# Kernel tuning notes

Hardware: AMD Instinct MI355X
Metric: run time of the kernel (lower is better)

## Reference

```python
import jax, jax.numpy as jnp
import numpy as np

IN_FF = 7  # joints
MASK = np.ones(9, dtype=np.float32)  # [P(3), RPY sin/cos (6)]


def _mlp(x, params):
    # params: list of (W, b); sigmoid after every layer except the last (predict)
    h = x
    for W, b in params[:-1]:
        h = jax.nn.sigmoid(h @ W + b)
    W, b = params[-1]
    return h @ W + b


def _rpy_head(x, params):
    # FeedForwardNet_RPY forward: y -> [sin(y0), cos(y1)], angle = atan2(sin, cos)
    y = _mlp(x, params)
    s = jnp.sin(y[..., 0])
    c = jnp.cos(y[..., 1])
    ang = jnp.arctan2(s, c)
    return jnp.stack([s, c, ang], axis=-1)  # (..., 3)


def setup_inputs():
    key = jax.random.key(0)
    ks = jax.random.split(key, 26)
    m = 16384
    d = {"x": jax.random.normal(ks[0], (m, 2 * IN_FF), jnp.float32)}

    def lin(k, fi, fo, name, i):
        k1, k2 = jax.random.split(k)
        lim = 1.0 / np.sqrt(fi)  # torch Linear default init
        d[name + "_W" + str(i)] = jax.random.uniform(k1, (fi, fo), jnp.float32, -lim, lim)
        d[name + "_b" + str(i)] = jax.random.uniform(k2, (fo,), jnp.float32, -lim, lim)

    idx = 1
    for name, dims in [("pos", [7, 512, 512, 3]), ("roll", [7, 256, 256, 2]),
                       ("pitch", [7, 256, 256, 2]), ("yaw", [7, 256, 256, 2])]:
        for i in range(3):
            lin(ks[idx], dims[i], dims[i + 1], name, i)
            idx += 1
    return d


def _forward(x, pos_p, roll_p, pitch_p, yaw_p):
    mask = jnp.asarray(MASK)
    M_P, M_RPY = mask[:3], mask[3:]
    q, qdot = x[:, :IN_FF], x[:, IN_FF:]

    # position net: forward + per-sample Jacobian (exact, replaces the autograd loop)
    P = _mlp(q, pos_p)                                          # (m, 3)
    J_P = jax.vmap(jax.jacfwd(lambda z: _mlp(z, pos_p)))(q)     # (m, 3, 7)
    vel = jnp.einsum("moi,mi->mo", J_P, qdot)                   # bmm(J_P, jointVels)
    P = P * M_P
    vel = vel * M_P

    heads = []
    for p in (roll_p, pitch_p, yaw_p):
        f = lambda z, p=p: _rpy_head(z, p)
        y = f(q)                                # (m, 3): [sin, cos, angle]
        J = jax.vmap(jax.jacfwd(f))(q)          # (m, 3, 7)
        v = jnp.einsum("moi,mi->mo", J[:, :2, :], qdot)  # (m, 2)
        heads.append((y, J, v))
    (yR, JR, vR), (yPi, JPi, vPi), (yY, JY, vY) = heads

    # order: [roll_sin, pitch_sin, yaw_sin, roll_cos, pitch_cos, yaw_cos]
    RPY = jnp.stack([yR[:, 0], yPi[:, 0], yY[:, 0], yR[:, 1], yPi[:, 1], yY[:, 1]], axis=1) * M_RPY
    vel_RPY = jnp.stack([vR[:, 0], vPi[:, 0], vY[:, 0], vR[:, 1], vPi[:, 1], vY[:, 1]], axis=1) * M_RPY
    J_RPY = jnp.stack([JR[:, 0], JPi[:, 0], JY[:, 0], JR[:, 1], JPi[:, 1], JY[:, 1]], axis=1)  # (m,6,7)

    out = jnp.concatenate([P, RPY, vel, vel_RPY], axis=1)            # (m, 18)
    J_tot = jnp.concatenate([J_P, J_RPY], axis=1)                    # (m, 9, 7)
    out_angles = jnp.concatenate([P, yR[:, 2:3], yPi[:, 2:3], yY[:, 2:3]], axis=1)       # (m, 6)
    J_tot_angles = jnp.concatenate([J_P, JR[:, 2:3], JPi[:, 2:3], JY[:, 2:3]], axis=1)   # (m, 6, 7)
    return out, J_tot, out_angles, J_tot_angles


def reference(x, pos_W0, pos_b0, pos_W1, pos_b1, pos_W2, pos_b2,
              roll_W0, roll_b0, roll_W1, roll_b1, roll_W2, roll_b2,
              pitch_W0, pitch_b0, pitch_W1, pitch_b1, pitch_W2, pitch_b2,
              yaw_W0, yaw_b0, yaw_W1, yaw_b1, yaw_W2, yaw_b2):
    pos_p = [(pos_W0, pos_b0), (pos_W1, pos_b1), (pos_W2, pos_b2)]
    roll_p = [(roll_W0, roll_b0), (roll_W1, roll_b1), (roll_W2, roll_b2)]
    pitch_p = [(pitch_W0, pitch_b0), (pitch_W1, pitch_b1), (pitch_W2, pitch_b2)]
    yaw_p = [(yaw_W0, yaw_b0), (yaw_W1, yaw_b1), (yaw_W2, yaw_b2)]
    return _forward(x, pos_p, roll_p, pitch_p, yaw_p)
```

## Files before the change

### kernel.cpp

```cpp
#include <hip/hip_runtime.h>
#include <math.h>

typedef __attribute__((ext_vector_type(8))) short short8;
typedef __attribute__((ext_vector_type(4))) float floatx4;
typedef __attribute__((ext_vector_type(2))) float floatx2;
typedef __attribute__((ext_vector_type(2))) unsigned uint2v;

__device__ __forceinline__ float sig(float z) { return 1.0f / (1.0f + __expf(-z)); }

__device__ __forceinline__ unsigned short f2bf(float f) {
    unsigned u = __float_as_uint(f);
    u = (u + 0x7FFFu + ((u >> 16) & 1u)) >> 16;
    return (unsigned short)u;
}

__device__ __forceinline__ unsigned cvtpk_bf16(float lo, float hi) {
    unsigned r;
    asm("v_cvt_pk_bf16_f32 %0, %1, %2" : "=v"(r) : "v"(lo), "v"(hi));
    return r;
}

__device__ __forceinline__ void st_pack4(unsigned short* p, float v0, float v1, float v2, float v3) {
    uint2v u;
    u.x = cvtpk_bf16(v0, v1);
    u.y = cvtpk_bf16(v2, v3);
    *(uint2v*)p = u;
}

__device__ __forceinline__ floatx2 fma2(floatx2 a, floatx2 b, floatx2 c) {
    return __builtin_elementwise_fma(a, b, c);
}

__global__ void convert_all(const float* __restrict__ s0, const float* __restrict__ s1,
                            const float* __restrict__ s2, const float* __restrict__ s3,
                            unsigned short* __restrict__ ws) {
    int idx = blockIdx.x * 256 + threadIdx.x;
    const float* src; unsigned short* dst; int H, logH, local;
    if (idx < 262144) { src = s0; dst = ws; H = 512; logH = 9; local = idx; }
    else {
        int r = idx - 262144; int m = r >> 16; local = r & 65535;
        H = 256; logH = 8;
        src = (m == 0) ? s1 : (m == 1) ? s2 : s3;
        dst = ws + 262144 + m * 65536;
    }
    int n = local & (H - 1), k = local >> logH;
    int KT = H >> 5;
    int blk = (n >> 4) * KT + (k >> 5);
    int lane = ((k >> 3) & 3) * 16 + (n & 15);
    int j = k & 7;
    dst[(blk * 64 + lane) * 8 + j] = f2bf(src[local]);
}

struct PosS {
    float B0[512], B1[512], W2[1536];
    float Q[4][8], Qd[4][8];
    float Sum[32][3];
};
struct RpyS {
    float B0[256], B1[256], W2[512];
    float Q[8][8], Qd[8][8];
    float Sum[64][2];
};

__global__ __launch_bounds__(256, 3)
void fused_mfma(const float* __restrict__ x,
                const float* __restrict__ pW0, const float* __restrict__ pb0,
                const float* __restrict__ pb1,
                const float* __restrict__ pW2, const float* __restrict__ pb2,
                const float* __restrict__ rW0_, const float* __restrict__ rb0_,
                const float* __restrict__ rb1_,
                const float* __restrict__ rW2_, const float* __restrict__ rb2_,
                const float* __restrict__ piW0, const float* __restrict__ pib0,
                const float* __restrict__ pib1,
                const float* __restrict__ piW2, const float* __restrict__ pib2,
                const float* __restrict__ yW0, const float* __restrict__ yb0,
                const float* __restrict__ yb1,
                const float* __restrict__ yW2, const float* __restrict__ yb2,
                const unsigned short* __restrict__ wsBase,
                float* __restrict__ out, int ns)
{
    extern __shared__ unsigned short sA[];
    __shared__ union { PosS p; RpyS r; } sU;

    const int tid = threadIdx.x;
    const int xcd  = blockIdx.x & 7;
    const int slot = blockIdx.x >> 3;
    const int o_l  = slot / 5, r5 = slot % 5;
    const int o = xcd + (o_l << 3);

    const size_t JTOT = (size_t)ns * 18, OUTA = (size_t)ns * 81, JANG = (size_t)ns * 87;
    const floatx4 z4 = {0.f, 0.f, 0.f, 0.f};
    const floatx2 z2v = {0.f, 0.f};
    const int w = tid >> 6, lane = tid & 63;
    const int quad = lane >> 4, col = lane & 15;
    const int srcl = lane & 47;
    const int lxk = lane ^ (quad << 1);

    if (r5 < 2) {
        const int m0 = (o * 2 + r5) * 4;
        const unsigned short* wsW1 = wsBase;

        const float b1r0 = pb1[tid], b1r1 = pb1[tid + 256];
        float w2r[6];
        #pragma unroll
        for (int t = 0; t < 6; ++t) w2r[t] = pW2[tid + 256 * t];

        for (int i = tid; i < 512; i += 256) sU.p.B0[i] = pb0[i];
        if (tid < 56) {
            int m = tid / 14, c = tid % 14;
            float v = x[(m0 + m) * 14 + c];
            if (c < 7) sU.p.Q[m][c] = v; else sU.p.Qd[m][c - 7] = v;
        }
        __syncthreads();

        const float4* W04 = (const float4*)pW0;

        floatx4 acc[2][8];
        #pragma unroll
        for (int rt = 0; rt < 2; rt++)
            #pragma unroll
            for (int ct = 0; ct < 8; ct++) acc[rt][ct] = z4;

        const short8* bbase = (const short8*)wsW1 + (size_t)(w * 8 * 16) * 64 + lane;
        short8 b0[4], b1[4], b2[4];

#define PLD(B, KT) { \
            B[0] = bbase[((cp4 + 0) * 16 + hh8 + (KT)) * 64]; \
            B[1] = bbase[((cp4 + 1) * 16 + hh8 + (KT)) * 64]; \
            B[2] = bbase[((cp4 + 2) * 16 + hh8 + (KT)) * 64]; \
            B[3] = bbase[((cp4 + 3) * 16 + hh8 + (KT)) * 64]; }
#define PST(B, KT) { \
            const short8 a0 = *(const short8*)&sA[(0 * 8 + (KT)) * 512 + (lxk ^ (KT)) * 8]; \
            const short8 a1 = *(const short8*)&sA[(1 * 8 + (KT)) * 512 + (lxk ^ (KT)) * 8]; \
            acc[0][cp4 + 0] = __builtin_amdgcn_mfma_f32_16x16x32_bf16(a0, B[0], acc[0][cp4 + 0], 0, 0, 0); \
            acc[1][cp4 + 0] = __builtin_amdgcn_mfma_f32_16x16x32_bf16(a1, B[0], acc[1][cp4 + 0], 0, 0, 0); \
            acc[0][cp4 + 1] = __builtin_amdgcn_mfma_f32_16x16x32_bf16(a0, B[1], acc[0][cp4 + 1], 0, 0, 0); \
            acc[1][cp4 + 1] = __builtin_amdgcn_mfma_f32_16x16x32_bf16(a1, B[1], acc[1][cp4 + 1], 0, 0, 0); \
            acc[0][cp4 + 2] = __builtin_amdgcn_mfma_f32_16x16x32_bf16(a0, B[2], acc[0][cp4 + 2], 0, 0, 0); \
            acc[1][cp4 + 2] = __builtin_amdgcn_mfma_f32_16x16x32_bf16(a1, B[2], acc[1][cp4 + 2], 0, 0, 0); \
            acc[0][cp4 + 3] = __builtin_amdgcn_mfma_f32_16x16x32_bf16(a0, B[3], acc[0][cp4 + 3], 0, 0, 0); \
            acc[1][cp4 + 3] = __builtin_amdgcn_mfma_f32_16x16x32_bf16(a1, B[3], acc[1][cp4 + 3], 0, 0, 0); }

        #pragma unroll
        for (int hh = 0; hh < 2; ++hh) {
            const int hh8 = hh * 8;
            b0[0] = bbase[(0 * 16 + hh8) * 64];
            b0[1] = bbase[(1 * 16 + hh8) * 64];
            b0[2] = bbase[(2 * 16 + hh8) * 64];
            b0[3] = bbase[(3 * 16 + hh8) * 64];
            {
                const int jh = tid & 1, item = tid >> 1;
                const int s = item >> 5, k8l = item & 31, k8 = (hh << 5) | k8l;
                float q[7]; floatx2 w0a[7], w0b[7];
                #pragma unroll
                for (int i = 0; i < 7; i++) {
                    q[i] = sU.p.Q[s][i];
                    float4 a = W04[i * 128 + k8 * 2 + jh];
                    w0a[i] = (floatx2){a.x, a.y};
                    w0b[i] = (floatx2){a.z, a.w};
                }
                const float* bb = &sU.p.B0[k8 * 8 + jh * 4];
                floatx2 za = {bb[0], bb[1]}, zb = {bb[2], bb[3]};
                #pragma unroll
                for (int i = 0; i < 7; i++) {
                    floatx2 qs = {q[i], q[i]};
                    za = fma2(qs, w0a[i], za);
                    zb = fma2(qs, w0b[i], zb);
                }
                floatx2 ha = {sig(za[0]), sig(za[1])};
                floatx2 hb = {sig(zb[0]), sig(zb[1])};
                floatx2 da = ha - ha * ha;
                floatx2 db = hb - hb * hb;
                const int ktl = k8l >> 2, kq = k8l & 3;
                const int kxr = (kq << 4) ^ (kq << 1) ^ ktl;
                const int rr0 = s * 8;
                st_pack4(&sA[((rr0 >> 4) * 8 + ktl) * 512 + (kxr ^ (rr0 & 15)) * 8 + jh * 4],
                         ha[0], ha[1], hb[0], hb[1]);
                #pragma unroll
                for (int i = 0; i < 7; i++) {
                    const int rr = rr0 + 1 + i;
                    floatx2 ta = da * w0a[i], tb = db * w0b[i];
                    st_pack4(&sA[((rr >> 4) * 8 + ktl) * 512 + (kxr ^ (rr & 15)) * 8 + jh * 4],
                             ta[0], ta[1], tb[0], tb[1]);
                }
            }
            __syncthreads();

            #pragma unroll
            for (int cp = 0; cp < 2; ++cp) {
                const int cp4 = cp * 4;
                if (cp) PLD(b0, 0);
                PLD(b1, 1); PLD(b2, 2);
                __builtin_amdgcn_s_setprio(1);
                PST(b0, 0); PLD(b0, 3);
                PST(b1, 1); PLD(b1, 4);
                PST(b2, 2); PLD(b2, 5);
                PST(b0, 3); PLD(b0, 6);
                PST(b1, 4); PLD(b1, 7);
                PST(b2, 5);
                PST(b0, 6);
                PST(b1, 7);
                __builtin_amdgcn_s_setprio(0);
            }
            if (hh == 0) __syncthreads();
        }
#undef PLD
#undef PST

        sU.p.B1[tid] = b1r0; sU.p.B1[tid + 256] = b1r1;
        #pragma unroll
        for (int t = 0; t < 6; ++t) sU.p.W2[tid + 256 * t] = w2r[t];
        __syncthreads();

        floatx2 epv[2][4]; float eps[2][4];
        #pragma unroll
        for (int a = 0; a < 2; a++) for (int b = 0; b < 4; b++) { epv[a][b] = z2v; eps[a][b] = 0.f; }

        #pragma unroll
        for (int ct = 0; ct < 8; ++ct) {
            const int n = w * 128 + ct * 16 + col;
            const float b1n = sU.p.B1[n];
            const floatx2 w201 = {sU.p.W2[n * 3], sU.p.W2[n * 3 + 1]};
            const float w22 = sU.p.W2[n * 3 + 2];
            #pragma unroll
            for (int rt = 0; rt < 2; ++rt) {
                float z2c = __shfl(acc[rt][ct][0], srcl);
                float h2 = sig(z2c + b1n);
                float d2 = h2 - h2 * h2;
                #pragma unroll
                for (int r = 0; r < 4; ++r) {
                    float gg = ((quad & 1) == 0 && r == 0) ? h2 : d2 * acc[rt][ct][r];
                    epv[rt][r] = fma2((floatx2){gg, gg}, w201, epv[rt][r]);
                    eps[rt][r] = fmaf(gg, w22, eps[rt][r]);
                }
            }
        }

        {
            float* pl = (float*)sA;
            #pragma unroll
            for (int rt = 0; rt < 2; ++rt)
                #pragma unroll
                for (int r = 0; r < 4; ++r) {
                    int row = rt * 16 + quad * 4 + r;
                    int base = ((w * 32 + row) * 3) * 17 + col;
                    pl[base]      = epv[rt][r][0];
                    pl[base + 17] = epv[rt][r][1];
                    pl[base + 34] = eps[rt][r];
                }
        }
        __syncthreads();

        if (tid < 96) {
            const float* pl = (const float*)sA;
            int row = tid / 3, j = tid % 3;
            float v = 0.f;
            #pragma unroll
            for (int ww = 0; ww < 4; ++ww) {
                const float* q = &pl[((ww * 32 + row) * 3 + j) * 17];
                #pragma unroll
                for (int c = 0; c < 16; ++c) v += q[c];
            }
            int s = row >> 3, i = row & 7;
            size_t M = m0 + s;
            if (i == 0) { v += pb2[j]; out[M * 18 + j] = v; out[OUTA + M * 6 + j] = v; }
            else        { out[JTOT + M * 63 + j * 7 + (i - 1)] = v;
                          out[JANG + M * 42 + j * 7 + (i - 1)] = v; }
            sU.p.Sum[row][j] = v;
        }
        __syncthreads();
        if (tid < 12) {
            int s = tid / 3, j = tid % 3;
            float vel = 0.f;
            #pragma unroll
            for (int i = 0; i < 7; i++) vel = fmaf(sU.p.Sum[s * 8 + 1 + i][j], sU.p.Qd[s][i], vel);
            out[(size_t)(m0 + s) * 18 + 9 + j] = vel;
        }
    } else {
        const int h = r5 - 2;
        const int m0 = o * 8;
        const float* W0 = (h == 0) ? rW0_ : (h == 1) ? piW0 : yW0;
        const float* b0p = (h == 0) ? rb0_ : (h == 1) ? pib0 : yb0;
        const float* b1p = (h == 0) ? rb1_ : (h == 1) ? pib1 : yb1;
        const float* W2 = (h == 0) ? rW2_ : (h == 1) ? piW2 : yW2;
        const float* b2p = (h == 0) ? rb2_ : (h == 1) ? pib2 : yb2;
        const unsigned short* wsW1 = wsBase + 262144 + h * 65536;

        const float b1r0 = b1p[tid];
        const float w2r0 = W2[tid], w2r1 = W2[tid + 256];

        if (tid < 256) sU.r.B0[tid] = b0p[tid];
        if (tid < 112) {
            int m = tid / 14, c = tid % 14;
            float v = x[(m0 + m) * 14 + c];
            if (c < 7) sU.r.Q[m][c] = v; else sU.r.Qd[m][c - 7] = v;
        }
        __syncthreads();

        const float4* W04 = (const float4*)W0;

        floatx4 acc[4][4];
        #pragma unroll
        for (int rt = 0; rt < 4; rt++)
            #pragma unroll
            for (int ct = 0; ct < 4; ct++) acc[rt][ct] = z4;

        const short8* bbase = (const short8*)wsW1 + (size_t)(w * 4 * 8) * 64 + lane;
        short8 b0[2], b1[2], b2[2];

#define RLD(B, KT) { \
            B[0] = bbase[((cp2 + 0) * 8 + hh4 + (KT)) * 64]; \
            B[1] = bbase[((cp2 + 1) * 8 + hh4 + (KT)) * 64]; }
#define RST(B, KT) { \
            const int sw_ = hh4 + (KT); \
            const short8 a0 = *(const short8*)&sA[(0 * 4 + (KT)) * 512 + (lxk ^ sw_) * 8]; \
            const short8 a1 = *(const short8*)&sA[(1 * 4 + (KT)) * 512 + (lxk ^ sw_) * 8]; \
            const short8 a2 = *(const short8*)&sA[(2 * 4 + (KT)) * 512 + (lxk ^ sw_) * 8]; \
            const short8 a3 = *(const short8*)&sA[(3 * 4 + (KT)) * 512 + (lxk ^ sw_) * 8]; \
            acc[0][cp2 + 0] = __builtin_amdgcn_mfma_f32_16x16x32_bf16(a0, B[0], acc[0][cp2 + 0], 0, 0, 0); \
            acc[1][cp2 + 0] = __builtin_amdgcn_mfma_f32_16x16x32_bf16(a1, B[0], acc[1][cp2 + 0], 0, 0, 0); \
            acc[2][cp2 + 0] = __builtin_amdgcn_mfma_f32_16x16x32_bf16(a2, B[0], acc[2][cp2 + 0], 0, 0, 0); \
            acc[3][cp2 + 0] = __builtin_amdgcn_mfma_f32_16x16x32_bf16(a3, B[0], acc[3][cp2 + 0], 0, 0, 0); \
            acc[0][cp2 + 1] = __builtin_amdgcn_mfma_f32_16x16x32_bf16(a0, B[1], acc[0][cp2 + 1], 0, 0, 0); \
            acc[1][cp2 + 1] = __builtin_amdgcn_mfma_f32_16x16x32_bf16(a1, B[1], acc[1][cp2 + 1], 0, 0, 0); \
            acc[2][cp2 + 1] = __builtin_amdgcn_mfma_f32_16x16x32_bf16(a2, B[1], acc[2][cp2 + 1], 0, 0, 0); \
            acc[3][cp2 + 1] = __builtin_amdgcn_mfma_f32_16x16x32_bf16(a3, B[1], acc[3][cp2 + 1], 0, 0, 0); }

        #pragma unroll
        for (int hh = 0; hh < 2; ++hh) {
            const int hh4 = hh * 4;
            b0[0] = bbase[(0 * 8 + hh4) * 64];
            b0[1] = bbase[(1 * 8 + hh4) * 64];
            {
                const int jh = tid & 1, item = tid >> 1;
                const int s = item >> 4, k8l = item & 15, k8 = (hh << 4) | k8l;
                float q[7]; floatx2 w0a[7], w0b[7];
                #pragma unroll
                for (int i = 0; i < 7; i++) {
                    q[i] = sU.r.Q[s][i];
                    float4 a = W04[i * 64 + k8 * 2 + jh];
                    w0a[i] = (floatx2){a.x, a.y};
                    w0b[i] = (floatx2){a.z, a.w};
                }
                const float* bb = &sU.r.B0[k8 * 8 + jh * 4];
                floatx2 za = {bb[0], bb[1]}, zb = {bb[2], bb[3]};
                #pragma unroll
                for (int i = 0; i < 7; i++) {
                    floatx2 qs = {q[i], q[i]};
                    za = fma2(qs, w0a[i], za);
                    zb = fma2(qs, w0b[i], zb);
                }
                floatx2 ha = {sig(za[0]), sig(za[1])};
                floatx2 hb = {sig(zb[0]), sig(zb[1])};
                floatx2 da = ha - ha * ha;
                floatx2 db = hb - hb * hb;
                const int ktl = k8l >> 2, kq = k8l & 3;
                const int sw = (hh << 2) | ktl;
                const int kxr = (kq << 4) ^ (kq << 1) ^ sw;
                const int rr0 = s * 8;
                st_pack4(&sA[((rr0 >> 4) * 4 + ktl) * 512 + (kxr ^ (rr0 & 15)) * 8 + jh * 4],
                         ha[0], ha[1], hb[0], hb[1]);
                #pragma unroll
                for (int i = 0; i < 7; i++) {
                    const int rr = rr0 + 1 + i;
                    floatx2 ta = da * w0a[i], tb = db * w0b[i];
                    st_pack4(&sA[((rr >> 4) * 4 + ktl) * 512 + (kxr ^ (rr & 15)) * 8 + jh * 4],
                             ta[0], ta[1], tb[0], tb[1]);
                }
            }
            __syncthreads();

            #pragma unroll
            for (int cp = 0; cp < 2; ++cp) {
                const int cp2 = cp * 2;
                if (cp) RLD(b0, 0);
                RLD(b1, 1); RLD(b2, 2);
                __builtin_amdgcn_s_setprio(1);
                RST(b0, 0); RLD(b0, 3);
                RST(b1, 1);
                RST(b2, 2);
                RST(b0, 3);
                __builtin_amdgcn_s_setprio(0);
            }
            if (hh == 0) __syncthreads();
        }
#undef RLD
#undef RST

        sU.r.B1[tid] = b1r0;
        sU.r.W2[tid] = w2r0; sU.r.W2[tid + 256] = w2r1;
        __syncthreads();

        floatx2 epv[4][4];
        #pragma unroll
        for (int a = 0; a < 4; a++) for (int b = 0; b < 4; b++) epv[a][b] = z2v;

        #pragma unroll
        for (int ct = 0; ct < 4; ++ct) {
            const int n = w * 64 + ct * 16 + col;
            const float b1n = sU.r.B1[n];
            const floatx2 w201 = {sU.r.W2[n * 2], sU.r.W2[n * 2 + 1]};
            #pragma unroll
            for (int rt = 0; rt < 4; ++rt) {
                float z2c = __shfl(acc[rt][ct][0], srcl);
                float h2 = sig(z2c + b1n);
                float d2 = h2 - h2 * h2;
                #pragma unroll
                for (int r = 0; r < 4; ++r) {
                    float gg = ((quad & 1) == 0 && r == 0) ? h2 : d2 * acc[rt][ct][r];
                    epv[rt][r] = fma2((floatx2){gg, gg}, w201, epv[rt][r]);
                }
            }
        }

        {
            float* pl = (float*)sA;
            #pragma unroll
            for (int rt = 0; rt < 4; ++rt)
                #pragma unroll
                for (int r = 0; r < 4; ++r) {
                    int row = rt * 16 + quad * 4 + r;
                    int base = ((w * 64 + row) * 2) * 17 + col;
                    pl[base]      = epv[rt][r][0];
                    pl[base + 17] = epv[rt][r][1];
                }
        }
        __syncthreads();

        if (tid < 128) {
            const float* pl = (const float*)sA;
            int row = tid >> 1, j = tid & 1;
            float v = 0.f;
            #pragma unroll
            for (int ww = 0; ww < 4; ++ww) {
                const float* q = &pl[((ww * 64 + row) * 2 + j) * 17];
                #pragma unroll
                for (int c = 0; c < 16; ++c) v += q[c];
            }
            if ((row & 7) == 0) v += b2p[j];
            sU.r.Sum[row][j] = v;
        }
        __syncthreads();

        if (tid < 8) {
            int s = tid;
            size_t M = m0 + s;
            float y0 = sU.r.Sum[s * 8][0], y1 = sU.r.Sum[s * 8][1];
            float sv = sinf(y0), cv = cosf(y1);
            out[M * 18 + 3 + h] = sv;
            out[M * 18 + 6 + h] = cv;
            out[OUTA + M * 6 + 3 + h] = atan2f(sv, cv);
            float f0 = cosf(y0), f1 = -sinf(y1);
            float inv = 1.0f / fmaf(sv, sv, cv * cv);
            float v0 = 0.f, v1 = 0.f;
            #pragma unroll
            for (int i = 0; i < 7; i++) {
                float r0 = f0 * sU.r.Sum[s * 8 + 1 + i][0];
                float r1 = f1 * sU.r.Sum[s * 8 + 1 + i][1];
                out[JTOT + M * 63 + (3 + h) * 7 + i] = r0;
                out[JTOT + M * 63 + (6 + h) * 7 + i] = r1;
                out[JANG + M * 42 + (3 + h) * 7 + i] = (cv * r0 - sv * r1) * inv;
                v0 = fmaf(r0, sU.r.Qd[s][i], v0);
                v1 = fmaf(r1, sU.r.Qd[s][i], v1);
            }
            out[M * 18 + 12 + h] = v0;
            out[M * 18 + 15 + h] = v1;
        }
    }
}

extern "C" void kernel_launch(void* const* d_in, const int* in_sizes, int n_in,
                              void* d_out, int out_size, void* d_ws, size_t ws_size,
                              hipStream_t stream) {
    (void)n_in; (void)out_size; (void)ws_size;
    const float* x = (const float*)d_in[0];
    float* out = (float*)d_out;
    unsigned short* ws = (unsigned short*)d_ws;
    const int ns = in_sizes[0] / 14;

    convert_all<<<dim3(1792), 256, 0, stream>>>(
        (const float*)d_in[3], (const float*)d_in[9],
        (const float*)d_in[15], (const float*)d_in[21], ws);

    fused_mfma<<<dim3((ns / 8) * 5), 256, 34816, stream>>>(
        x,
        (const float*)d_in[1],  (const float*)d_in[2],  (const float*)d_in[4],
        (const float*)d_in[5],  (const float*)d_in[6],
        (const float*)d_in[7],  (const float*)d_in[8],  (const float*)d_in[10],
        (const float*)d_in[11], (const float*)d_in[12],
        (const float*)d_in[13], (const float*)d_in[14], (const float*)d_in[16],
        (const float*)d_in[17], (const float*)d_in[18],
        (const float*)d_in[19], (const float*)d_in[20], (const float*)d_in[22],
        (const float*)d_in[23], (const float*)d_in[24],
        ws, out, ns);
}
```

Before: 280.3 us.

## Raise occupancy to 4 blocks/SM by reusing sA for epilogue constants and shrinking prefetch

Moves the layer-1 bias and output-weight staging arrays out of the static shared union into the dynamic sA region after the MFMA loop finishes. An extra barrier protects the later partial-sum writes that alias the same space. This shrinks static LDS. The B-operand prefetch drops from triple to double buffering to cut register use, and launch bounds rise from 3 to 4 waves per SIMD. The aim is higher occupancy, at the cost of a shallower load-ahead distance and one more barrier.

```diff
diff --git a/kernel.cpp b/kernel.cpp
--- a/kernel.cpp
+++ b/kernel.cpp
@@ -52,17 +52,17 @@
 }
 
 struct PosS {
-    float B0[512], B1[512], W2[1536];
+    float B0[512];
     float Q[4][8], Qd[4][8];
     float Sum[32][3];
 };
 struct RpyS {
-    float B0[256], B1[256], W2[512];
+    float B0[256];
     float Q[8][8], Qd[8][8];
     float Sum[64][2];
 };
 
-__global__ __launch_bounds__(256, 3)
+__global__ __launch_bounds__(256, 4)
 void fused_mfma(const float* __restrict__ x,
                 const float* __restrict__ pW0, const float* __restrict__ pb0,
                 const float* __restrict__ pb1,
@@ -99,6 +99,8 @@
     if (r5 < 2) {
         const int m0 = (o * 2 + r5) * 4;
         const unsigned short* wsW1 = wsBase;
+        float* dB1 = (float*)(sA + 8192);
+        float* dW2 = (float*)(sA + 9216);
 
         const float b1r0 = pb1[tid], b1r1 = pb1[tid + 256];
         float w2r[6];
@@ -122,7 +124,7 @@
             for (int ct = 0; ct < 8; ct++) acc[rt][ct] = z4;
 
         const short8* bbase = (const short8*)wsW1 + (size_t)(w * 8 * 16) * 64 + lane;
-        short8 b0[4], b1[4], b2[4];
+        short8 b0[4], b1[4];
 
 #define PLD(B, KT) { \
             B[0] = bbase[((cp4 + 0) * 16 + hh8 + (KT)) * 64]; \
@@ -190,14 +192,14 @@
             for (int cp = 0; cp < 2; ++cp) {
                 const int cp4 = cp * 4;
                 if (cp) PLD(b0, 0);
-                PLD(b1, 1); PLD(b2, 2);
+                PLD(b1, 1);
                 __builtin_amdgcn_s_setprio(1);
-                PST(b0, 0); PLD(b0, 3);
-                PST(b1, 1); PLD(b1, 4);
-                PST(b2, 2); PLD(b2, 5);
-                PST(b0, 3); PLD(b0, 6);
-                PST(b1, 4); PLD(b1, 7);
-                PST(b2, 5);
+                PST(b0, 0); PLD(b0, 2);
+                PST(b1, 1); PLD(b1, 3);
+                PST(b0, 2); PLD(b0, 4);
+                PST(b1, 3); PLD(b1, 5);
+                PST(b0, 4); PLD(b0, 6);
+                PST(b1, 5); PLD(b1, 7);
                 PST(b0, 6);
                 PST(b1, 7);
                 __builtin_amdgcn_s_setprio(0);
@@ -207,9 +209,9 @@
 #undef PLD
 #undef PST
 
-        sU.p.B1[tid] = b1r0; sU.p.B1[tid + 256] = b1r1;
-        #pragma unroll
-        for (int t = 0; t < 6; ++t) sU.p.W2[tid + 256 * t] = w2r[t];
+        dB1[tid] = b1r0; dB1[tid + 256] = b1r1;
+        #pragma unroll
+        for (int t = 0; t < 6; ++t) dW2[tid + 256 * t] = w2r[t];
         __syncthreads();
 
         floatx2 epv[2][4]; float eps[2][4];
@@ -219,9 +221,9 @@
         #pragma unroll
         for (int ct = 0; ct < 8; ++ct) {
             const int n = w * 128 + ct * 16 + col;
-            const float b1n = sU.p.B1[n];
-            const floatx2 w201 = {sU.p.W2[n * 3], sU.p.W2[n * 3 + 1]};
-            const float w22 = sU.p.W2[n * 3 + 2];
+            const float b1n = dB1[n];
+            const floatx2 w201 = {dW2[n * 3], dW2[n * 3 + 1]};
+            const float w22 = dW2[n * 3 + 2];
             #pragma unroll
             for (int rt = 0; rt < 2; ++rt) {
                 float z2c = __shfl(acc[rt][ct][0], srcl);
@@ -235,6 +237,7 @@
                 }
             }
         }
+        __syncthreads();
 
         {
             float* pl = (float*)sA;
@@ -285,6 +288,8 @@
         const float* W2 = (h == 0) ? rW2_ : (h == 1) ? piW2 : yW2;
         const float* b2p = (h == 0) ? rb2_ : (h == 1) ? pib2 : yb2;
         const unsigned short* wsW1 = wsBase + 262144 + h * 65536;
+        float* dB1 = (float*)(sA + 8192);
+        float* dW2 = (float*)(sA + 8704);
 
         const float b1r0 = b1p[tid];
         const float w2r0 = W2[tid], w2r1 = W2[tid + 256];
@@ -306,7 +311,7 @@
             for (int ct = 0; ct < 4; ct++) acc[rt][ct] = z4;
 
         const short8* bbase = (const short8*)wsW1 + (size_t)(w * 4 * 8) * 64 + lane;
-        short8 b0[2], b1[2], b2[2];
+        short8 b0[2], b1[2];
 
 #define RLD(B, KT) { \
             B[0] = bbase[((cp2 + 0) * 8 + hh4 + (KT)) * 64]; \
@@ -374,12 +379,12 @@
             for (int cp = 0; cp < 2; ++cp) {
                 const int cp2 = cp * 2;
                 if (cp) RLD(b0, 0);
-                RLD(b1, 1); RLD(b2, 2);
+                RLD(b1, 1);
                 __builtin_amdgcn_s_setprio(1);
-                RST(b0, 0); RLD(b0, 3);
-                RST(b1, 1);
-                RST(b2, 2);
-                RST(b0, 3);
+                RST(b0, 0); RLD(b0, 2);
+                RST(b1, 1); RLD(b1, 3);
+                RST(b0, 2);
+                RST(b1, 3);
                 __builtin_amdgcn_s_setprio(0);
             }
             if (hh == 0) __syncthreads();
@@ -387,8 +392,8 @@
 #undef RLD
 #undef RST
 
-        sU.r.B1[tid] = b1r0;
-        sU.r.W2[tid] = w2r0; sU.r.W2[tid + 256] = w2r1;
+        dB1[tid] = b1r0;
+        dW2[tid] = w2r0; dW2[tid + 256] = w2r1;
         __syncthreads();
 
         floatx2 epv[4][4];
@@ -398,8 +403,8 @@
         #pragma unroll
         for (int ct = 0; ct < 4; ++ct) {
             const int n = w * 64 + ct * 16 + col;
-            const float b1n = sU.r.B1[n];
-            const floatx2 w201 = {sU.r.W2[n * 2], sU.r.W2[n * 2 + 1]};
+            const float b1n = dB1[n];
+            const floatx2 w201 = {dW2[n * 2], dW2[n * 2 + 1]};
             #pragma unroll
             for (int rt = 0; rt < 4; ++rt) {
                 float z2c = __shfl(acc[rt][ct][0], srcl);
@@ -412,6 +417,7 @@
                 }
             }
         }
+        __syncthreads();
 
         {
             float* pl = (float*)sA;
```

Result: slower. 333.7 us (+19.0%).
